# Optimization experiments

Measured on AMD Instinct MI355X. Metric: run time of the kernel, lower is better.

The kernel has to match this reference:

```python
import jax, jax.numpy as jnp
import numpy as np

N_NODES = 100000
N_EDGES = 800000
NODE_DIM = 128
EDGE_DIM = 32
MSG_DIM = 128
EPS = 1e-5


def layer_norm(x, g, b):
    mu = jnp.mean(x, axis=-1, keepdims=True)
    var = jnp.var(x, axis=-1, keepdims=True)
    return (x - mu) * jax.lax.rsqrt(var + EPS) * g + b


def he_normal(key, shape):
    # kaiming_normal_ with nonlinearity='relu': std = sqrt(2 / fan_in)
    fan_in = shape[1]
    return jax.random.normal(key, shape, dtype=jnp.float32) * np.sqrt(2.0 / fan_in)


def setup_inputs() -> dict:
    key = jax.random.key(0)
    ks = jax.random.split(key, 8)
    nodes = jax.random.normal(ks[0], (N_NODES, NODE_DIM), dtype=jnp.float32)
    edge_index = jax.random.randint(ks[1], (2, N_EDGES), 0, N_NODES, dtype=jnp.int64)
    edge_attr = jax.random.normal(ks[2], (N_EDGES, EDGE_DIM), dtype=jnp.float32)
    # torch Linear weights are [out, in]
    W_message = he_normal(ks[3], (MSG_DIM, NODE_DIM + EDGE_DIM))
    W_node = he_normal(ks[4], (NODE_DIM, NODE_DIM))
    W1 = he_normal(ks[5], (NODE_DIM, NODE_DIM + MSG_DIM))
    b1 = jnp.zeros((NODE_DIM,), dtype=jnp.float32)
    ln1_g = jnp.ones((NODE_DIM,), dtype=jnp.float32)
    ln1_b = jnp.zeros((NODE_DIM,), dtype=jnp.float32)
    W2 = he_normal(ks[6], (NODE_DIM, NODE_DIM))
    b2 = jnp.zeros((NODE_DIM,), dtype=jnp.float32)
    ln2_g = jnp.ones((NODE_DIM,), dtype=jnp.float32)
    ln2_b = jnp.zeros((NODE_DIM,), dtype=jnp.float32)
    ln_g = jnp.ones((NODE_DIM,), dtype=jnp.float32)
    ln_b = jnp.zeros((NODE_DIM,), dtype=jnp.float32)
    return {"nodes": nodes, "edge_index": edge_index, "edge_attr": edge_attr,
            "W_message": W_message, "W_node": W_node,
            "W1": W1, "b1": b1, "ln1_g": ln1_g, "ln1_b": ln1_b,
            "W2": W2, "b2": b2, "ln2_g": ln2_g, "ln2_b": ln2_b,
            "ln_g": ln_g, "ln_b": ln_b}


def reference(nodes, edge_index, edge_attr, W_message, W_node,
              W1, b1, ln1_g, ln1_b, W2, b2, ln2_g, ln2_b, ln_g, ln_b):
    senders, receivers = edge_index[0], edge_index[1]
    n_nodes = nodes.shape[0]
    # gather -> linear
    sender_features = nodes[senders]                                  # [E, node_dim]
    message_input = jnp.concatenate([sender_features, edge_attr], -1)  # [E, node_dim+edge_dim]
    messages = message_input @ W_message.T                            # [E, msg_dim]
    # scatter sum aggregation
    aggregated = jax.ops.segment_sum(messages, receivers, num_segments=n_nodes)
    # node MLP (two Linear+ReLU+LayerNorm blocks)
    node_input = jnp.concatenate([nodes, aggregated], -1)             # [N, node_dim+msg_dim]
    h = layer_norm(jax.nn.relu(node_input @ W1.T + b1), ln1_g, ln1_b)
    node_out = layer_norm(jax.nn.relu(h @ W2.T + b2), ln2_g, ln2_b)
    # residual + final LayerNorm
    return layer_norm(nodes @ W_node.T + node_out, ln_g, ln_b)
```

## Files before the change

### kernel.cpp

```cpp
#include <hip/hip_runtime.h>
#include <math.h>


#define THREADS 256
#define BM 64
#define BK 32
#define APB 40
#define BP 132

typedef __attribute__((ext_vector_type(8))) short bf16x8;
typedef __attribute__((ext_vector_type(4))) float f32x4;

struct GemmSmem {
  unsigned short As[BM][APB];
  unsigned short Bs[128][APB];
};
struct EpiSmem {
  float Cs[BM][BP];
  float psum[BM][4];
  float psq[BM][4];
  float mu[BM];
  float rs[BM];
};
union NodeSmem { GemmSmem g; EpiSmem e; };

union BF8 { bf16x8 v; ushort4 q[2]; };

__device__ __forceinline__ unsigned short f2bf(float x) {
  union { float f; unsigned u; } c; c.f = x;
  unsigned u = c.u;
  u += 0x7fffu + ((u >> 16) & 1u);
  return (unsigned short)(u >> 16);
}
__device__ __forceinline__ float bf2f(unsigned h) {
  union { unsigned u; float f; } c; c.u = h << 16; return c.f;
}
__device__ __forceinline__ ushort4 cvt4(float4 v) {
  ushort4 p; p.x = f2bf(v.x); p.y = f2bf(v.y); p.z = f2bf(v.z); p.w = f2bf(v.w);
  return p;
}

__global__ __launch_bounds__(256) void prep_kernel(
    const float* __restrict__ W1, const float* __restrict__ Wm,
    const float* __restrict__ W2, const float* __restrict__ Wn,
    const float* __restrict__ nodes, const int* __restrict__ eidx,
    unsigned short* __restrict__ Wcat, unsigned short* __restrict__ W2b,
    unsigned short* __restrict__ Wnb, unsigned short* __restrict__ nodes_bf,
    int* __restrict__ counts, int Nn, int E, int nconv) {
  const int b = blockIdx.x, tid = threadIdx.x;
  if (b < 128) {
    for (int t = tid; t < 288; t += 256) {
      float v;
      if (t < 128) {
        v = W1[(size_t)b * 256 + t];
      } else {
        int u = t - 128;
        float s = 0.f;
#pragma unroll 8
        for (int k = 0; k < 128; ++k)
          s += W1[(size_t)b * 256 + 128 + k] * Wm[(size_t)k * 160 + u];
        v = s;
      }
      Wcat[(size_t)b * 288 + t] = f2bf(v);
    }
  } else if (b < 144) {
    int idx = (b - 128) * 1024 + tid * 4;
    *(ushort4*)&W2b[idx] = cvt4(*(const float4*)&W2[idx]);
  } else if (b < 160) {
    int idx = (b - 144) * 1024 + tid * 4;
    *(ushort4*)&Wnb[idx] = cvt4(*(const float4*)&Wn[idx]);
  } else if (b < 160 + nconv) {
    int idx = ((b - 160) * 256 + tid) * 4;
    if (idx < Nn * 128)
      *(ushort4*)&nodes_bf[idx] = cvt4(*(const float4*)&nodes[idx]);
  } else {
    int i = (b - 160 - nconv) * 256 + tid;
    if (i < E) atomicAdd(&counts[eidx[E + i]], 1);
  }
}

__global__ __launch_bounds__(256) void scan1_kernel(const int* __restrict__ counts,
                                                    int* __restrict__ bsum, int Nn) {
  __shared__ int red[256];
  const int tid = threadIdx.x;
  int base = blockIdx.x * 2048 + tid * 8;
  int s = 0;
#pragma unroll
  for (int i = 0; i < 8; ++i) {
    int idx = base + i;
    if (idx < Nn) s += counts[idx];
  }
  red[tid] = s;
  __syncthreads();
#pragma unroll
  for (int off = 128; off; off >>= 1) {
    if (tid < off) red[tid] += red[tid + off];
    __syncthreads();
  }
  if (tid == 0) bsum[blockIdx.x] = red[0];
}

__global__ __launch_bounds__(256) void scan2_kernel(const int* __restrict__ bsum,
                                                    int* __restrict__ boff, int NB) {
  __shared__ int arr[256];
  const int tid = threadIdx.x;
  int v = (tid < NB) ? bsum[tid] : 0;
  arr[tid] = v;
  __syncthreads();
  for (int off = 1; off < 256; off <<= 1) {
    int t2 = (tid >= off) ? arr[tid - off] : 0;
    __syncthreads();
    arr[tid] += t2;
    __syncthreads();
  }
  if (tid < NB) boff[tid] = arr[tid] - v;
}

__global__ __launch_bounds__(256) void scan3_kernel(const int* __restrict__ counts,
                                                    const int* __restrict__ boff,
                                                    int* __restrict__ row_ptr,
                                                    int* __restrict__ cursor, int Nn) {
  __shared__ int arr[256];
  const int tid = threadIdx.x;
  int base = blockIdx.x * 2048 + tid * 8;
  int c[8];
  int s = 0;
#pragma unroll
  for (int i = 0; i < 8; ++i) {
    int idx = base + i;
    c[i] = (idx < Nn) ? counts[idx] : 0;
    s += c[i];
  }
  arr[tid] = s;
  __syncthreads();
  for (int off = 1; off < 256; off <<= 1) {
    int t2 = (tid >= off) ? arr[tid - off] : 0;
    __syncthreads();
    arr[tid] += t2;
    __syncthreads();
  }
  int run = arr[tid] - s + boff[blockIdx.x];
#pragma unroll
  for (int i = 0; i < 8; ++i) {
    int idx = base + i;
    if (idx < Nn) {
      row_ptr[idx] = run;
      cursor[idx] = run;
    }
    run += c[i];
  }
}

__global__ __launch_bounds__(256) void build_kernel(const int* __restrict__ eidx,
                                                    int* __restrict__ cursor,
                                                    int* __restrict__ perm,
                                                    int* __restrict__ snds, int E) {
  int i = blockIdx.x * 256 + threadIdx.x;
  if (i < E) {
    int r = eidx[E + i];
    int pos = atomicAdd(&cursor[r], 1);
    perm[pos] = i;
    snds[pos] = eidx[i];
  }
}

__global__ __launch_bounds__(256) void aggsum_kernel(
    const unsigned short* __restrict__ nodes_bf, const float* __restrict__ eattr,
    const int* __restrict__ row_ptr, const int* __restrict__ rend,
    const int* __restrict__ perm, const int* __restrict__ snds,
    unsigned short* __restrict__ S, int Nn) {
  const int wid = blockIdx.x * 4 + (threadIdx.x >> 6);
  if (wid >= Nn) return;
  const int lane = threadIdx.x & 63;
  const int start = row_ptr[wid];
  const int end = rend[wid];
  const int deg = end - start;
  const int dmax = deg < 64 ? deg : 64;

  int sv = 0, pv = 0;
  if (lane < deg) {
    sv = snds[start + lane];
    pv = perm[start + lane];
  }

  const unsigned* nodes32 = (const unsigned*)nodes_bf;
  const int rsub = lane >> 5;
  const int col = lane & 31;
  float s0 = 0.f, s1 = 0.f, seA = 0.f, seB = 0.f;

  int t = 0;
  for (; t + 4 <= dmax; t += 4) {
    int i0 = __shfl(sv, t + 0);
    int i1 = __shfl(sv, t + 1);
    int i2 = __shfl(sv, t + 2);
    int i3 = __shfl(sv, t + 3);
    int pA = __shfl(pv, t + rsub);
    int pB = __shfl(pv, t + 2 + rsub);
    unsigned a0 = nodes32[(size_t)i0 * 64 + lane];
    unsigned a1 = nodes32[(size_t)i1 * 64 + lane];
    unsigned a2 = nodes32[(size_t)i2 * 64 + lane];
    unsigned a3 = nodes32[(size_t)i3 * 64 + lane];
    float vA = eattr[(size_t)pA * 32 + col];
    float vB = eattr[(size_t)pB * 32 + col];
    s0 += bf2f(a0 & 0xffffu) + bf2f(a1 & 0xffffu) +
          bf2f(a2 & 0xffffu) + bf2f(a3 & 0xffffu);
    s1 += bf2f(a0 >> 16) + bf2f(a1 >> 16) + bf2f(a2 >> 16) + bf2f(a3 >> 16);
    seA += vA;
    seB += vB;
  }
  for (; t < dmax; ++t) {
    int i0 = __shfl(sv, t);
    int p = __shfl(pv, t);
    unsigned a0 = nodes32[(size_t)i0 * 64 + lane];
    s0 += bf2f(a0 & 0xffffu);
    s1 += bf2f(a0 >> 16);
    if (rsub == 0) seA += eattr[(size_t)p * 32 + col];
  }
  for (int j = start + 64; j < end; ++j) {
    int sI = snds[j];
    int p = perm[j];
    unsigned a = nodes32[(size_t)sI * 64 + lane];
    s0 += bf2f(a & 0xffffu);
    s1 += bf2f(a >> 16);
    if (rsub == 0) seA += eattr[(size_t)p * 32 + col];
  }

  float se = seA + seB;
  se += __shfl_xor(se, 32);

  unsigned pack = (unsigned)f2bf(s0) | ((unsigned)f2bf(s1) << 16);
  ((unsigned*)S)[(size_t)wid * 80 + lane] = pack;

  float lo = __shfl(se, 2 * (lane & 15));
  float hi = __shfl(se, 2 * (lane & 15) + 1);
  if (lane < 16) {
    unsigned p2 = (unsigned)f2bf(lo) | ((unsigned)f2bf(hi) << 16);
    ((unsigned*)S)[(size_t)wid * 80 + 64 + lane] = p2;
  }
}

__device__ __forceinline__ void gemm_chunk(const GemmSmem& sm, int tid,
                                           f32x4 acc[2][4]) {
  const int lane = tid & 63;
  const int quad = lane >> 4;
  const int lm = lane & 15;
  const int wid = tid >> 6;
  const int wy = wid >> 1, wx = wid & 1;

  bf16x8 af[2], bf[4];
#pragma unroll
  for (int mt = 0; mt < 2; ++mt)
    af[mt] = *(const bf16x8*)&sm.As[32 * wy + 16 * mt + lm][quad * 8];
#pragma unroll
  for (int nt = 0; nt < 4; ++nt)
    bf[nt] = *(const bf16x8*)&sm.Bs[64 * wx + 16 * nt + lm][quad * 8];
#pragma unroll
  for (int mt = 0; mt < 2; ++mt)
#pragma unroll
    for (int nt = 0; nt < 4; ++nt)
      acc[mt][nt] = __builtin_amdgcn_mfma_f32_16x16x32_bf16(
          af[mt], bf[nt], acc[mt][nt], 0, 0, 0);
}

__device__ __forceinline__ void gemm_k128(const unsigned short* __restrict__ A,
                                          const unsigned short* __restrict__ W,
                                          int row0, int Nn, GemmSmem& g, int tid,
                                          f32x4 acc[2][4]) {
  for (int kc = 0; kc < 128; kc += BK) {
    {
      int r = tid >> 2, u = tid & 3;
      int row = row0 + r;
      if (row >= Nn) row = Nn - 1;
      BF8 t;
      t.v = *(const bf16x8*)&A[(size_t)row * 128 + kc + 8 * u];
      *(ushort4*)&g.As[r][8 * u] = t.q[0];
      *(ushort4*)&g.As[r][8 * u + 4] = t.q[1];
    }
#pragma unroll
    for (int c = 0; c < 2; ++c) {
      int f = tid + 256 * c;
      int n = f >> 2, u = f & 3;
      BF8 t;
      t.v = *(const bf16x8*)&W[(size_t)n * 128 + kc + 8 * u];
      *(ushort4*)&g.Bs[n][8 * u] = t.q[0];
      *(ushort4*)&g.Bs[n][8 * u + 4] = t.q[1];
    }
    __syncthreads();
    gemm_chunk(g, tid, acc);
    __syncthreads();
  }
}

__device__ __forceinline__ void ln_stats(EpiSmem& e, int tid) {
  {
    int q = tid & 3, r = tid >> 2;
    float s = 0.f, s2 = 0.f;
#pragma unroll 8
    for (int j = q * 32; j < q * 32 + 32; ++j) {
      float x = e.Cs[r][j];
      s += x;
      s2 += x * x;
    }
    e.psum[r][q] = s;
    e.psq[r][q] = s2;
  }
  __syncthreads();
  if (tid < BM) {
    float S_ = 0.f, S2 = 0.f;
#pragma unroll
    for (int q = 0; q < 4; ++q) {
      S_ += e.psum[tid][q];
      S2 += e.psq[tid][q];
    }
    float m = S_ * (1.f / 128.f);
    float var = S2 * (1.f / 128.f) - m * m;
    e.mu[tid] = m;
    e.rs[tid] = rsqrtf(var + 1e-5f);
  }
  __syncthreads();
}

__global__ __launch_bounds__(THREADS, 4) void node0_kernel(
    const unsigned short* __restrict__ A0, const unsigned short* __restrict__ A1,
    const unsigned short* __restrict__ Wb, const float* __restrict__ bias,
    const float* __restrict__ g, const float* __restrict__ bln,
    unsigned short* __restrict__ outb, int Nn) {
  __shared__ NodeSmem sm;
  const int tid = threadIdx.x;
  const int row0 = blockIdx.x * BM;

  f32x4 acc[2][4];
#pragma unroll
  for (int mt = 0; mt < 2; ++mt)
#pragma unroll
    for (int nt = 0; nt < 4; ++nt) acc[mt][nt] = (f32x4)0.f;

  for (int kc = 0; kc < 288; kc += BK) {
    {
      int r = tid >> 2, u = tid & 3;
      int k = kc + 8 * u;
      int row = row0 + r;
      if (row >= Nn) row = Nn - 1;
      BF8 t;
      if (kc >= 128)
        t.v = *(const bf16x8*)&A1[(size_t)row * 160 + (k - 128)];
      else
        t.v = *(const bf16x8*)&A0[(size_t)row * 128 + k];
      *(ushort4*)&sm.g.As[r][8 * u] = t.q[0];
      *(ushort4*)&sm.g.As[r][8 * u + 4] = t.q[1];
    }
#pragma unroll
    for (int c = 0; c < 2; ++c) {
      int f = tid + 256 * c;
      int n = f >> 2, u = f & 3;
      BF8 t;
      t.v = *(const bf16x8*)&Wb[(size_t)n * 288 + kc + 8 * u];
      *(ushort4*)&sm.g.Bs[n][8 * u] = t.q[0];
      *(ushort4*)&sm.g.Bs[n][8 * u + 4] = t.q[1];
    }
    __syncthreads();
    gemm_chunk(sm.g, tid, acc);
    __syncthreads();
  }

  const int lane = tid & 63;
  const int quad = lane >> 4;
  const int lm = lane & 15;
  const int wid = tid >> 6;
  const int wy = wid >> 1, wx = wid & 1;

  float bval[4];
#pragma unroll
  for (int nt = 0; nt < 4; ++nt) bval[nt] = bias[64 * wx + 16 * nt + lm];
#pragma unroll
  for (int mt = 0; mt < 2; ++mt)
#pragma unroll
    for (int i = 0; i < 4; ++i) {
      int r = 32 * wy + 16 * mt + quad * 4 + i;
#pragma unroll
      for (int nt = 0; nt < 4; ++nt) {
        int col = 64 * wx + 16 * nt + lm;
        sm.e.Cs[r][col] = fmaxf(acc[mt][nt][i] + bval[nt], 0.f);
      }
    }
  __syncthreads();
  ln_stats(sm.e, tid);

#pragma unroll 4
  for (int s = 0; s < 32; ++s) {
    int flat = tid + THREADS * s;
    int r = flat >> 7, j = flat & 127;
    int row = row0 + r;
    if (row < Nn) {
      float x = sm.e.Cs[r][j];
      outb[(size_t)row * 128 + j] =
          f2bf((x - sm.e.mu[r]) * sm.e.rs[r] * g[j] + bln[j]);
    }
  }
}

__global__ __launch_bounds__(THREADS, 3) void node12_kernel(
    const unsigned short* __restrict__ h_bf,
    const unsigned short* __restrict__ nodes_bf,
    const unsigned short* __restrict__ W2b, const unsigned short* __restrict__ Wnb,
    const float* __restrict__ b2, const float* __restrict__ g2,
    const float* __restrict__ bl2, const float* __restrict__ gf,
    const float* __restrict__ blf, float* __restrict__ out, int Nn) {
  __shared__ GemmSmem g;
  __shared__ EpiSmem e;
  const int tid = threadIdx.x;
  const int row0 = blockIdx.x * BM;
  const int lane = tid & 63;
  const int quad = lane >> 4;
  const int lm = lane & 15;
  const int wid = tid >> 6;
  const int wy = wid >> 1, wx = wid & 1;

  f32x4 acc[2][4];
#pragma unroll
  for (int mt = 0; mt < 2; ++mt)
#pragma unroll
    for (int nt = 0; nt < 4; ++nt) acc[mt][nt] = (f32x4)0.f;

  gemm_k128(h_bf, W2b, row0, Nn, g, tid, acc);

  float bval[4];
#pragma unroll
  for (int nt = 0; nt < 4; ++nt) bval[nt] = b2[64 * wx + 16 * nt + lm];
#pragma unroll
  for (int mt = 0; mt < 2; ++mt)
#pragma unroll
    for (int i = 0; i < 4; ++i) {
      int r = 32 * wy + 16 * mt + quad * 4 + i;
#pragma unroll
      for (int nt = 0; nt < 4; ++nt) {
        int col = 64 * wx + 16 * nt + lm;
        e.Cs[r][col] = fmaxf(acc[mt][nt][i] + bval[nt], 0.f);
      }
    }
  __syncthreads();
  ln_stats(e, tid);

#pragma unroll 4
  for (int s = 0; s < 32; ++s) {
    int flat = tid + THREADS * s;
    int r = flat >> 7, j = flat & 127;
    float x = e.Cs[r][j];
    e.Cs[r][j] = (x - e.mu[r]) * e.rs[r] * g2[j] + bl2[j];
  }
  __syncthreads();

#pragma unroll
  for (int mt = 0; mt < 2; ++mt)
#pragma unroll
    for (int nt = 0; nt < 4; ++nt) acc[mt][nt] = (f32x4)0.f;

  gemm_k128(nodes_bf, Wnb, row0, Nn, g, tid, acc);

#pragma unroll
  for (int mt = 0; mt < 2; ++mt)
#pragma unroll
    for (int i = 0; i < 4; ++i) {
      int r = 32 * wy + 16 * mt + quad * 4 + i;
#pragma unroll
      for (int nt = 0; nt < 4; ++nt) {
        int col = 64 * wx + 16 * nt + lm;
        e.Cs[r][col] = acc[mt][nt][i] + e.Cs[r][col];
      }
    }
  __syncthreads();
  ln_stats(e, tid);

#pragma unroll 4
  for (int s = 0; s < 32; ++s) {
    int flat = tid + THREADS * s;
    int r = flat >> 7, j = flat & 127;
    int row = row0 + r;
    if (row < Nn) {
      float x = e.Cs[r][j];
      out[(size_t)row * 128 + j] =
          (x - e.mu[r]) * e.rs[r] * gf[j] + blf[j];
    }
  }
}

extern "C" void kernel_launch(void* const* d_in, const int* in_sizes, int n_in,
                              void* d_out, int out_size, void* d_ws, size_t ws_size,
                              hipStream_t stream) {
  const float* nodes = (const float*)d_in[0];
  const int* eidx    = (const int*)d_in[1];
  const float* eattr = (const float*)d_in[2];
  const float* Wm    = (const float*)d_in[3];
  const float* Wn    = (const float*)d_in[4];
  const float* W1    = (const float*)d_in[5];
  const float* b1    = (const float*)d_in[6];
  const float* g1    = (const float*)d_in[7];
  const float* bl1   = (const float*)d_in[8];
  const float* W2    = (const float*)d_in[9];
  const float* b2    = (const float*)d_in[10];
  const float* g2    = (const float*)d_in[11];
  const float* bl2   = (const float*)d_in[12];
  const float* gf    = (const float*)d_in[13];
  const float* blf   = (const float*)d_in[14];
  float* out = (float*)d_out;

  const int Nn = in_sizes[0] / 128;
  const int E  = in_sizes[2] / 32;

  int* counts  = (int*)d_ws;
  int* row_ptr = counts + Nn;
  int* cursor  = row_ptr + Nn;
  int* bsum    = cursor + Nn;
  int* boff    = bsum + 256;
  int* perm    = boff + 256;
  int* snds    = perm + E;
  unsigned short* Wcat     = (unsigned short*)(snds + E);
  unsigned short* W2b      = Wcat + 128 * 288;
  unsigned short* Wnb      = W2b + 128 * 128;
  unsigned short* nodes_bf = Wnb + 128 * 128;
  unsigned short* h_bf     = nodes_bf + (size_t)Nn * 128;
  unsigned short* S_bf     = h_bf + (size_t)Nn * 128;

  hipMemsetAsync(counts, 0, (size_t)Nn * sizeof(int), stream);

  const int nconv = (Nn * 32 + 255) / 256;
  const int nhist = (E + 255) / 256;
  const int NB = (Nn + 2047) / 2048;
  const int ngrid = (Nn + BM - 1) / BM;

  prep_kernel<<<160 + nconv + nhist, 256, 0, stream>>>(
      W1, Wm, W2, Wn, nodes, eidx, Wcat, W2b, Wnb, nodes_bf, counts, Nn, E, nconv);
  scan1_kernel<<<NB, 256, 0, stream>>>(counts, bsum, Nn);
  scan2_kernel<<<1, 256, 0, stream>>>(bsum, boff, NB);
  scan3_kernel<<<NB, 256, 0, stream>>>(counts, boff, row_ptr, cursor, Nn);
  build_kernel<<<nhist, 256, 0, stream>>>(eidx, cursor, perm, snds, E);
  aggsum_kernel<<<(Nn + 3) / 4, 256, 0, stream>>>(nodes_bf, eattr, row_ptr, cursor,
                                                  perm, snds, S_bf, Nn);
  node0_kernel<<<ngrid, THREADS, 0, stream>>>(nodes_bf, S_bf, Wcat, b1, g1, bl1,
                                              h_bf, Nn);
  node12_kernel<<<ngrid, THREADS, 0, stream>>>(h_bf, nodes_bf, W2b, Wnb, b2, g2,
                                               bl2, gf, blf, out, Nn);
}
```

Baseline: 448.2 us.

## Fuse node MLP first block into second kernel, keep hidden activations in LDS

Merges node0 and node12 into one kernel so the first Linear+ReLU+LayerNorm output stays in shared memory as fp32 and is converted to bf16 on the fly while it is staged for the W2 GEMM. This removes the h_bf global write and read-back plus one kernel launch. In exchange the fused kernel uses separate GEMM and epilogue shared buffers and is limited to 3 blocks per CU instead of 4 for the first GEMM, which may reduce occupancy.

```diff
diff --git a/kernel.cpp b/kernel.cpp
--- a/kernel.cpp
+++ b/kernel.cpp
@@ -22,7 +22,6 @@
   float mu[BM];
   float rs[BM];
 };
-union NodeSmem { GemmSmem g; EpiSmem e; };
 
 union BF8 { bf16x8 v; ushort4 q[2]; };
 
@@ -291,6 +290,33 @@
   }
 }
 
+__device__ __forceinline__ void gemm_k128_lds(const EpiSmem& e,
+                                              const unsigned short* __restrict__ W,
+                                              GemmSmem& g, int tid,
+                                              f32x4 acc[2][4]) {
+  for (int kc = 0; kc < 128; kc += BK) {
+    {
+      int r = tid >> 2, u = tid & 3;
+      float4 lo = *(const float4*)&e.Cs[r][kc + 8 * u];
+      float4 hi = *(const float4*)&e.Cs[r][kc + 8 * u + 4];
+      *(ushort4*)&g.As[r][8 * u] = cvt4(lo);
+      *(ushort4*)&g.As[r][8 * u + 4] = cvt4(hi);
+    }
+#pragma unroll
+    for (int c = 0; c < 2; ++c) {
+      int f = tid + 256 * c;
+      int n = f >> 2, u = f & 3;
+      BF8 t;
+      t.v = *(const bf16x8*)&W[(size_t)n * 128 + kc + 8 * u];
+      *(ushort4*)&g.Bs[n][8 * u] = t.q[0];
+      *(ushort4*)&g.Bs[n][8 * u + 4] = t.q[1];
+    }
+    __syncthreads();
+    gemm_chunk(g, tid, acc);
+    __syncthreads();
+  }
+}
+
 __device__ __forceinline__ void ln_stats(EpiSmem& e, int tid) {
   {
     int q = tid & 3, r = tid >> 2;
@@ -320,88 +346,10 @@
   __syncthreads();
 }
 
-__global__ __launch_bounds__(THREADS, 4) void node0_kernel(
+__global__ __launch_bounds__(THREADS, 3) void node_fused_kernel(
     const unsigned short* __restrict__ A0, const unsigned short* __restrict__ A1,
-    const unsigned short* __restrict__ Wb, const float* __restrict__ bias,
-    const float* __restrict__ g, const float* __restrict__ bln,
-    unsigned short* __restrict__ outb, int Nn) {
-  __shared__ NodeSmem sm;
-  const int tid = threadIdx.x;
-  const int row0 = blockIdx.x * BM;
-
-  f32x4 acc[2][4];
-#pragma unroll
-  for (int mt = 0; mt < 2; ++mt)
-#pragma unroll
-    for (int nt = 0; nt < 4; ++nt) acc[mt][nt] = (f32x4)0.f;
-
-  for (int kc = 0; kc < 288; kc += BK) {
-    {
-      int r = tid >> 2, u = tid & 3;
-      int k = kc + 8 * u;
-      int row = row0 + r;
-      if (row >= Nn) row = Nn - 1;
-      BF8 t;
-      if (kc >= 128)
-        t.v = *(const bf16x8*)&A1[(size_t)row * 160 + (k - 128)];
-      else
-        t.v = *(const bf16x8*)&A0[(size_t)row * 128 + k];
-      *(ushort4*)&sm.g.As[r][8 * u] = t.q[0];
-      *(ushort4*)&sm.g.As[r][8 * u + 4] = t.q[1];
-    }
-#pragma unroll
-    for (int c = 0; c < 2; ++c) {
-      int f = tid + 256 * c;
-      int n = f >> 2, u = f & 3;
-      BF8 t;
-      t.v = *(const bf16x8*)&Wb[(size_t)n * 288 + kc + 8 * u];
-      *(ushort4*)&sm.g.Bs[n][8 * u] = t.q[0];
-      *(ushort4*)&sm.g.Bs[n][8 * u + 4] = t.q[1];
-    }
-    __syncthreads();
-    gemm_chunk(sm.g, tid, acc);
-    __syncthreads();
-  }
-
-  const int lane = tid & 63;
-  const int quad = lane >> 4;
-  const int lm = lane & 15;
-  const int wid = tid >> 6;
-  const int wy = wid >> 1, wx = wid & 1;
-
-  float bval[4];
-#pragma unroll
-  for (int nt = 0; nt < 4; ++nt) bval[nt] = bias[64 * wx + 16 * nt + lm];
-#pragma unroll
-  for (int mt = 0; mt < 2; ++mt)
-#pragma unroll
-    for (int i = 0; i < 4; ++i) {
-      int r = 32 * wy + 16 * mt + quad * 4 + i;
-#pragma unroll
-      for (int nt = 0; nt < 4; ++nt) {
-        int col = 64 * wx + 16 * nt + lm;
-        sm.e.Cs[r][col] = fmaxf(acc[mt][nt][i] + bval[nt], 0.f);
-      }
-    }
-  __syncthreads();
-  ln_stats(sm.e, tid);
-
-#pragma unroll 4
-  for (int s = 0; s < 32; ++s) {
-    int flat = tid + THREADS * s;
-    int r = flat >> 7, j = flat & 127;
-    int row = row0 + r;
-    if (row < Nn) {
-      float x = sm.e.Cs[r][j];
-      outb[(size_t)row * 128 + j] =
-          f2bf((x - sm.e.mu[r]) * sm.e.rs[r] * g[j] + bln[j]);
-    }
-  }
-}
-
-__global__ __launch_bounds__(THREADS, 3) void node12_kernel(
-    const unsigned short* __restrict__ h_bf,
-    const unsigned short* __restrict__ nodes_bf,
+    const unsigned short* __restrict__ Wcat, const float* __restrict__ b1,
+    const float* __restrict__ g1, const float* __restrict__ bl1,
     const unsigned short* __restrict__ W2b, const unsigned short* __restrict__ Wnb,
     const float* __restrict__ b2, const float* __restrict__ g2,
     const float* __restrict__ bl2, const float* __restrict__ gf,
@@ -422,25 +370,86 @@
 #pragma unroll
     for (int nt = 0; nt < 4; ++nt) acc[mt][nt] = (f32x4)0.f;
 
-  gemm_k128(h_bf, W2b, row0, Nn, g, tid, acc);
-
-  float bval[4];
-#pragma unroll
-  for (int nt = 0; nt < 4; ++nt) bval[nt] = b2[64 * wx + 16 * nt + lm];
+  for (int kc = 0; kc < 288; kc += BK) {
+    {
+      int r = tid >> 2, u = tid & 3;
+      int k = kc + 8 * u;
+      int row = row0 + r;
+      if (row >= Nn) row = Nn - 1;
+      BF8 t;
+      if (kc >= 128)
+        t.v = *(const bf16x8*)&A1[(size_t)row * 160 + (k - 128)];
+      else
+        t.v = *(const bf16x8*)&A0[(size_t)row * 128 + k];
+      *(ushort4*)&g.As[r][8 * u] = t.q[0];
+      *(ushort4*)&g.As[r][8 * u + 4] = t.q[1];
+    }
+#pragma unroll
+    for (int c = 0; c < 2; ++c) {
+      int f = tid + 256 * c;
+      int n = f >> 2, u = f & 3;
+      BF8 t;
+      t.v = *(const bf16x8*)&Wcat[(size_t)n * 288 + kc + 8 * u];
+      *(ushort4*)&g.Bs[n][8 * u] = t.q[0];
+      *(ushort4*)&g.Bs[n][8 * u + 4] = t.q[1];
+    }
+    __syncthreads();
+    gemm_chunk(g, tid, acc);
+    __syncthreads();
+  }
+
+  {
+    float bval[4];
+#pragma unroll
+    for (int nt = 0; nt < 4; ++nt) bval[nt] = b1[64 * wx + 16 * nt + lm];
+#pragma unroll
+    for (int mt = 0; mt < 2; ++mt)
+#pragma unroll
+      for (int i = 0; i < 4; ++i) {
+        int r = 32 * wy + 16 * mt + quad * 4 + i;
+#pragma unroll
+        for (int nt = 0; nt < 4; ++nt) {
+          int col = 64 * wx + 16 * nt + lm;
+          e.Cs[r][col] = fmaxf(acc[mt][nt][i] + bval[nt], 0.f);
+        }
+      }
+  }
+  __syncthreads();
+  ln_stats(e, tid);
+#pragma unroll 4
+  for (int s = 0; s < 32; ++s) {
+    int flat = tid + THREADS * s;
+    int r = flat >> 7, j = flat & 127;
+    float x = e.Cs[r][j];
+    e.Cs[r][j] = (x - e.mu[r]) * e.rs[r] * g1[j] + bl1[j];
+  }
+  __syncthreads();
+
 #pragma unroll
   for (int mt = 0; mt < 2; ++mt)
 #pragma unroll
-    for (int i = 0; i < 4; ++i) {
-      int r = 32 * wy + 16 * mt + quad * 4 + i;
-#pragma unroll
-      for (int nt = 0; nt < 4; ++nt) {
-        int col = 64 * wx + 16 * nt + lm;
-        e.Cs[r][col] = fmaxf(acc[mt][nt][i] + bval[nt], 0.f);
+    for (int nt = 0; nt < 4; ++nt) acc[mt][nt] = (f32x4)0.f;
+
+  gemm_k128_lds(e, W2b, g, tid, acc);
+
+  {
+    float bval[4];
+#pragma unroll
+    for (int nt = 0; nt < 4; ++nt) bval[nt] = b2[64 * wx + 16 * nt + lm];
+#pragma unroll
+    for (int mt = 0; mt < 2; ++mt)
+#pragma unroll
+      for (int i = 0; i < 4; ++i) {
+        int r = 32 * wy + 16 * mt + quad * 4 + i;
+#pragma unroll
+        for (int nt = 0; nt < 4; ++nt) {
+          int col = 64 * wx + 16 * nt + lm;
+          e.Cs[r][col] = fmaxf(acc[mt][nt][i] + bval[nt], 0.f);
+        }
       }
-    }
+  }
   __syncthreads();
   ln_stats(e, tid);
-
 #pragma unroll 4
   for (int s = 0; s < 32; ++s) {
     int flat = tid + THREADS * s;
@@ -455,7 +464,7 @@
 #pragma unroll
     for (int nt = 0; nt < 4; ++nt) acc[mt][nt] = (f32x4)0.f;
 
-  gemm_k128(nodes_bf, Wnb, row0, Nn, g, tid, acc);
+  gemm_k128(A0, Wnb, row0, Nn, g, tid, acc);
 
 #pragma unroll
   for (int mt = 0; mt < 2; ++mt)
@@ -518,8 +527,7 @@
   unsigned short* W2b      = Wcat + 128 * 288;
   unsigned short* Wnb      = W2b + 128 * 128;
   unsigned short* nodes_bf = Wnb + 128 * 128;
-  unsigned short* h_bf     = nodes_bf + (size_t)Nn * 128;
-  unsigned short* S_bf     = h_bf + (size_t)Nn * 128;
+  unsigned short* S_bf     = nodes_bf + (size_t)Nn * 128;
 
   hipMemsetAsync(counts, 0, (size_t)Nn * sizeof(int), stream);
 
@@ -536,8 +544,6 @@
   build_kernel<<<nhist, 256, 0, stream>>>(eidx, cursor, perm, snds, E);
   aggsum_kernel<<<(Nn + 3) / 4, 256, 0, stream>>>(nodes_bf, eattr, row_ptr, cursor,
                                                   perm, snds, S_bf, Nn);
-  node0_kernel<<<ngrid, THREADS, 0, stream>>>(nodes_bf, S_bf, Wcat, b1, g1, bl1,
-                                              h_bf, Nn);
-  node12_kernel<<<ngrid, THREADS, 0, stream>>>(h_bf, nodes_bf, W2b, Wnb, b2, g2,
-                                               bl2, gf, blf, out, Nn);
-}
+  node_fused_kernel<<<ngrid, THREADS, 0, stream>>>(
+      nodes_bf, S_bf, Wcat, b1, g1, bl1, W2b, Wnb, b2, g2, bl2, gf, blf, out, Nn);
+}
```

New measurement: 425.9 us. 1.05x faster.
